# Optimization experiments

Hardware: AMD Instinct MI355X
Metric: run time of the kernel (lower is better)

Reference implementation:

```python
import jax, jax.numpy as jnp
import numpy as np

B, NELEC, D, NION = 2048, 32, 512, 8
NSPIN = 2
N = NELEC // NSPIN  # electrons per spin = orbital-matrix size = 16


def setup_inputs() -> dict:
    key = jax.random.key(0)
    ks = jax.random.split(key, 6)
    eq_inputs = jax.random.normal(ks[0], (B, NELEC, D), jnp.float32)
    r_ei = jax.random.normal(ks[1], (B, NELEC, NION, 3), jnp.float32)
    # learned params (stacked over the 2 spins; equal split so shapes match)
    W_lin = jax.random.normal(ks[2], (NSPIN, 2 * D, N), jnp.float32) * (0.5 / np.sqrt(D))
    b_lin = jax.random.normal(ks[3], (NSPIN, N), jnp.float32) * 0.1
    A_env = jax.random.normal(ks[4], (NSPIN, 3, 3, NION, N), jnp.float32) * 0.3
    w_ion = jax.random.normal(ks[5], (NSPIN, NION, N), jnp.float32)
    return dict(eq_inputs=eq_inputs, r_ei=r_ei, W_lin=W_lin, b_lin=b_lin,
                A_env=A_env, w_ion=w_ion)


def reference(eq_inputs, r_ei, W_lin, b_lin, A_env, w_ion):
    """Per-particle determinant antiequivariance layer.

    For each spin s and particle p, a doubly-equivariant orbital matrix
    M_p[j, k] = (y_p . W1[:,k] + y_j . W2[:,k] + b[k]) * env[j, k]
    is built (pair-concat dense split into two einsums to avoid the (B,n,n,2d)
    intermediate), with anisotropic exponential envelopes
    env[j, k] = sum_I w_ion[I,k] * exp(-||A[:,:,I,k] @ r_ei[j,I,:]||).
    Output per spin: y_p * det(M_p), stacked over spins -> (B, 2, n, d).
    """
    b, nelec, d = eq_inputs.shape
    n = nelec // NSPIN
    x = eq_inputs.reshape(b, NSPIN, n, d)            # spin_split=2 equal split
    r = r_ei.reshape(b, NSPIN, n, r_ei.shape[-2], 3)
    W1, W2 = W_lin[:, :d], W_lin[:, d:]
    # linear (doubly equivariant) part: (B, S, n_p, n_j, n_k)
    lin_p = jnp.einsum('bspf,sfk->bspk', x, W1)
    lin_j = jnp.einsum('bsjf,sfk->bsjk', x, W2) + b_lin[None, :, None, :]
    lin = lin_p[:, :, :, None, :] + lin_j[:, :, None, :, :]
    # anisotropic exponential envelopes: exp(-||A (r - R)||), combined over ions
    ar = jnp.einsum('bsjip,spqik->bsjiqk', r, A_env)        # (B,S,n,I,3,k)
    env = jnp.exp(-jnp.sqrt(jnp.sum(ar * ar, axis=-2)))     # (B,S,n,I,k)
    env = jnp.einsum('bsjik,sik->bsjk', env, w_ion)         # (B,S,n_j,n_k)
    M = lin * env[:, :, None, :, :]                         # (B,S,n_p,n_j,n_k)
    dets = jnp.linalg.det(M)                                # (B,S,n_p)
    # y_p * det(M_p), per spin (stacked over the spin axis)
    return x * dets[..., None]                              # (B,S,n,d)
```

## Files before the change

kernel.cpp:

```cpp
#include <hip/hip_runtime.h>
#include <hip/hip_bf16.h>
#include <cstdint>
#include <cstddef>

#define NSPIN 2
#define NPART 16
#define DDIM  512
#define NION  8

#define WSLICE     976
#define LDS_FLOATS (4 * WSLICE)
#define LDS_BYTES  (LDS_FLOATS * 4)

#define WS_GRAM_F  16384

typedef short bf16x8 __attribute__((ext_vector_type(8)));
typedef float f32x4  __attribute__((ext_vector_type(4)));

__device__ __forceinline__ short bfc(float x) {
    unsigned u = __float_as_uint(x);
    u += 0x7FFFu + ((u >> 16) & 1u);
    return (short)(u >> 16);
}

union AFU { bf16x8 v; __hip_bfloat162 h[4]; };

__device__ __forceinline__ bf16x8 cvt8(const float4& a, const float4& b) {
    AFU u;
    u.h[0] = __float22bfloat162_rn(make_float2(a.x, a.y));
    u.h[1] = __float22bfloat162_rn(make_float2(a.z, a.w));
    u.h[2] = __float22bfloat162_rn(make_float2(b.x, b.y));
    u.h[3] = __float22bfloat162_rn(make_float2(b.z, b.w));
    return u.v;
}

#define DPPMAXU(k, ctrl) { unsigned o_ = (unsigned)__builtin_amdgcn_update_dpp(0, (int)(k), (ctrl), 0xF, 0xF, true); (k) = (k) > o_ ? (k) : o_; }

__global__ void __launch_bounds__(256)
prep_kernel(const float* __restrict__ WL, const float* __restrict__ AE,
            const float* __restrict__ WI, float* __restrict__ WSF)
{
    const int t = threadIdx.x;
    if (blockIdx.x < 16) {
        int slot = blockIdx.x * 256 + t;
        int spin = slot >> 11;
        int rem  = slot & 2047;
        int half = rem >> 10;
        int ks   = (rem >> 6) & 15;
        int lane = rem & 63;
        int cc2  = lane & 15, hh = lane >> 4;
        const float* src = WL + (size_t)spin * (2 * DDIM * NPART)
                         + ((size_t)(half * 512 + ks * 32 + hh * 8)) * NPART + cc2;
        ushort u[8];
        #pragma unroll
        for (int e = 0; e < 8; ++e) u[e] = (ushort)bfc(src[e * NPART]);
        uint4 pk;
        pk.x = (unsigned)u[0] | ((unsigned)u[1] << 16);
        pk.y = (unsigned)u[2] | ((unsigned)u[3] << 16);
        pk.z = (unsigned)u[4] | ((unsigned)u[5] << 16);
        pk.w = (unsigned)u[6] | ((unsigned)u[7] << 16);
        ((uint4*)WSF)[slot] = pk;
    } else {
        int s  = t >> 7;
        int ke = (t >> 3) & 15;
        int i  = t & 7;
        const float* Ag = AE + (size_t)s * (9 * NION * NPART);
        float a00 = Ag[((0 * 3 + 0) * NION + i) * NPART + ke];
        float a01 = Ag[((0 * 3 + 1) * NION + i) * NPART + ke];
        float a02 = Ag[((0 * 3 + 2) * NION + i) * NPART + ke];
        float a10 = Ag[((1 * 3 + 0) * NION + i) * NPART + ke];
        float a11 = Ag[((1 * 3 + 1) * NION + i) * NPART + ke];
        float a12 = Ag[((1 * 3 + 2) * NION + i) * NPART + ke];
        float a20 = Ag[((2 * 3 + 0) * NION + i) * NPART + ke];
        float a21 = Ag[((2 * 3 + 1) * NION + i) * NPART + ke];
        float a22 = Ag[((2 * 3 + 2) * NION + i) * NPART + ke];
        float* g = WSF + WS_GRAM_F + t * 8;
        g[0] = a00 * a00 + a01 * a01 + a02 * a02;
        g[1] = a10 * a10 + a11 * a11 + a12 * a12;
        g[2] = a20 * a20 + a21 * a21 + a22 * a22;
        g[3] = a00 * a10 + a01 * a11 + a02 * a12;
        g[4] = a00 * a20 + a01 * a21 + a02 * a22;
        g[5] = a10 * a20 + a11 * a21 + a12 * a22;
        g[6] = WI[(size_t)s * (NION * NPART) + i * NPART + ke];
        g[7] = 0.f;
    }
}

__global__ void __launch_bounds__(256, 4)
ppdet_kernel(const float* __restrict__ EQ, const float* __restrict__ RE,
             const float* __restrict__ WSF, const float* __restrict__ BL,
             float* __restrict__ OUT)
{
    extern __shared__ float ls[];
    const int t  = threadIdx.x;
    const int s  = blockIdx.x >> 9;
    const int b0 = (blockIdx.x & 511) * 4;

    const int l  = t & 63;
    const int w  = t >> 6;
    const int b  = b0 + w;
    const int c  = l & 15;
    const int h4 = l >> 4;
    const int jr = l & 15;
    const int g  = l >> 4;

    float* wls = ls + w * WSLICE;

    {
        const float* xg  = EQ + ((size_t)(b * 32 + s * 16 + c)) * DDIM + h4 * 8;
        const uint4* wb1 = (const uint4*)WSF + (size_t)s * 2048;
        const uint4* wb2 = wb1 + 1024;
        f32x4 accp = {0.f, 0.f, 0.f, 0.f}, accj = {0.f, 0.f, 0.f, 0.f};
        #pragma unroll
        for (int kb = 0; kb < 4; ++kb) {
            float4 xa[8];
            uint4 w1v[4], w2v[4];
            #pragma unroll
            for (int u = 0; u < 4; ++u) {
                xa[2 * u]     = *(const float4*)(xg + (kb * 4 + u) * 32);
                xa[2 * u + 1] = *(const float4*)(xg + (kb * 4 + u) * 32 + 4);
                w1v[u] = wb1[(kb * 4 + u) * 64 + l];
                w2v[u] = wb2[(kb * 4 + u) * 64 + l];
            }
            #pragma unroll
            for (int u = 0; u < 4; ++u) {
                bf16x8 af = cvt8(xa[2 * u], xa[2 * u + 1]);
                accp = __builtin_amdgcn_mfma_f32_16x16x32_bf16(af, *(bf16x8*)&w1v[u], accp, 0, 0, 0);
                accj = __builtin_amdgcn_mfma_f32_16x16x32_bf16(af, *(bf16x8*)&w2v[u], accj, 0, 0, 0);
            }
        }
        const float blv = BL[s * NPART + c];
        #pragma unroll
        for (int q = 0; q < 4; ++q) {
            wls[(h4 * 4 + q) * 20 + c]        = accp[q];
            wls[320 + (h4 * 4 + q) * 20 + c]  = accj[q] + blv;
        }
    }

    {
        float rr[24];
        const float* rrow = RE + ((size_t)(b * 32 + s * 16 + jr)) * 24;
        #pragma unroll
        for (int m = 0; m < 6; ++m) {
            float4 v = ((const float4*)rrow)[m];
            rr[m * 4 + 0] = v.x; rr[m * 4 + 1] = v.y;
            rr[m * 4 + 2] = v.z; rr[m * 4 + 3] = v.w;
        }
        #pragma unroll
        for (int kx = 0; kx < 4; ++kx) {
            const int ke2 = g + kx * 4;
            const float4* gp = (const float4*)(WSF + WS_GRAM_F + s * 1024 + ke2 * 64);
            float ev = 0.f;
            #pragma unroll
            for (int i = 0; i < 8; ++i) {
                float4 gA = gp[2 * i];
                float4 gB = gp[2 * i + 1];
                float r0 = rr[i * 3 + 0], r1 = rr[i * 3 + 1], r2 = rr[i * 3 + 2];
                float ss = r0 * r0 * gA.x;
                ss = fmaf(r1 * r1, gA.y, ss);
                ss = fmaf(r2 * r2, gA.z, ss);
                float tcr = r0 * r1 * gA.w;
                tcr = fmaf(r0 * r2, gB.x, tcr);
                tcr = fmaf(r1 * r2, gB.y, tcr);
                ss = fmaf(2.f, tcr, ss);
                ss = fmaxf(ss, 0.f);
                ev = fmaf(gB.z, __expf(-__builtin_amdgcn_sqrtf(ss)), ev);
            }
            wls[640 + jr * 20 + ke2] = ev;
        }
    }

    asm volatile("s_waitcnt lgkmcnt(0)" ::: "memory");

    const int lanebase4 = (l & 48) << 2;
    #pragma unroll 1
    for (int pp = 0; pp < 4; ++pp) {
        const int p = pp * 4 + g;
        float Mr[16];
        const float* lp = wls + p * 20;
        const float* lj = wls + 320 + jr * 20;
        const float* ev = wls + 640 + jr * 20;
        #pragma unroll
        for (int cq = 0; cq < 4; ++cq) {
            float4 a  = *(const float4*)(lp + cq * 4);
            float4 bb = *(const float4*)(lj + cq * 4);
            float4 e  = *(const float4*)(ev + cq * 4);
            Mr[cq * 4 + 0] = (a.x + bb.x) * e.x;
            Mr[cq * 4 + 1] = (a.y + bb.y) * e.y;
            Mr[cq * 4 + 2] = (a.z + bb.z) * e.z;
            Mr[cq * 4 + 3] = (a.w + bb.w) * e.w;
        }
        float detv = 1.f;
        unsigned sel = 0u;
        int inv = 0;
        bool msel = false;
        #pragma unroll
        for (int cc = 0; cc < 16; ++cc) {
            unsigned key = msel ? 0u
                : ((__float_as_uint(fabsf(Mr[cc])) & 0xFFFFFFF0u) | (unsigned)jr);
            DPPMAXU(key, 0x121); DPPMAXU(key, 0x122); DPPMAXU(key, 0x124); DPPMAXU(key, 0x128);
            const int idx = (int)(key & 15u);
            const bool ispiv = (jr == idx) && !msel;
            const int srcaddr = lanebase4 | (idx << 2);
            float Pr[16];
            #pragma unroll
            for (int k2 = cc; k2 < 16; ++k2)
                Pr[k2] = __int_as_float(__builtin_amdgcn_ds_bpermute(
                             srcaddr, __float_as_int(Mr[k2])));
            const float pv = Pr[cc];
            const float f = (msel || ispiv || pv == 0.f) ? 0.f
                          : Mr[cc] * __builtin_amdgcn_rcpf(pv);
            inv += __popc(sel >> (idx + 1));
            sel |= (1u << idx);
            msel = msel || ispiv;
            detv *= pv;
            #pragma unroll
            for (int k2 = cc + 1; k2 < 16; ++k2)
                Mr[k2] = fmaf(-f, Pr[k2], Mr[k2]);
        }
        if (inv & 1) detv = -detv;
        if (jr == 0) wls[960 + p] = detv;
    }

    asm volatile("s_waitcnt lgkmcnt(0)" ::: "memory");

    {
        const size_t base = ((size_t)(b * 32 + s * 16)) * DDIM;
        const f32x4* src4 = (const f32x4*)(EQ + base);
        f32x4* dst4 = (f32x4*)(OUT + base);
        #pragma unroll
        for (int i2 = 0; i2 < 32; ++i2) {
            int f4i = i2 * 64 + l;
            float dt = wls[960 + (f4i >> 7)];
            f32x4 xv = src4[f4i];
            f32x4 o = xv * dt;
            __builtin_nontemporal_store(o, dst4 + f4i);
        }
    }
}

extern "C" void kernel_launch(void* const* d_in, const int* in_sizes, int n_in,
                              void* d_out, int out_size, void* d_ws, size_t ws_size,
                              hipStream_t stream) {
    const float* EQ = (const float*)d_in[0];
    const float* RE = (const float*)d_in[1];
    const float* WL = (const float*)d_in[2];
    const float* BL = (const float*)d_in[3];
    const float* AE = (const float*)d_in[4];
    const float* WI = (const float*)d_in[5];
    float* OUT = (float*)d_out;
    float* WSF = (float*)d_ws;
    (void)in_sizes; (void)n_in; (void)out_size; (void)ws_size;

    prep_kernel<<<dim3(17), dim3(256), 0, stream>>>(WL, AE, WI, WSF);
    ppdet_kernel<<<dim3(1024), dim3(256), LDS_BYTES, stream>>>(EQ, RE, WSF, BL, OUT);
}
```

Baseline: 83.53 us.

## Split determinant computation and output scaling into separate kernels

The fused kernel is split in two. The first computes the per-particle determinants and writes them to workspace, and a second fully parallel kernel streams the inputs and scales them into the output. The aim is to decouple the latency-bound elimination phase from the bandwidth-bound scale phase so each gets a better launch shape. The cost is an extra kernel launch and a second full read of the 64MB input, since the fused version could reuse input data that was likely still in cache.

After: 105.8 us. 1.27x slower.

```diff
diff --git a/kernel.cpp b/kernel.cpp
--- a/kernel.cpp
+++ b/kernel.cpp
@@ -13,6 +13,7 @@
 #define LDS_BYTES  (LDS_FLOATS * 4)
 
 #define WS_GRAM_F  16384
+#define WS_DETS_F  18432
 
 typedef short bf16x8 __attribute__((ext_vector_type(8)));
 typedef float f32x4  __attribute__((ext_vector_type(4)));
@@ -87,9 +88,9 @@
 }
 
 __global__ void __launch_bounds__(256, 4)
-ppdet_kernel(const float* __restrict__ EQ, const float* __restrict__ RE,
-             const float* __restrict__ WSF, const float* __restrict__ BL,
-             float* __restrict__ OUT)
+dets_kernel(const float* __restrict__ EQ, const float* __restrict__ RE,
+            const float* __restrict__ WSF, const float* __restrict__ BL,
+            float* __restrict__ DETS)
 {
     extern __shared__ float ls[];
     const int t  = threadIdx.x;
@@ -219,23 +220,24 @@
                 Mr[k2] = fmaf(-f, Pr[k2], Mr[k2]);
         }
         if (inv & 1) detv = -detv;
-        if (jr == 0) wls[960 + p] = detv;
-    }
-
-    asm volatile("s_waitcnt lgkmcnt(0)" ::: "memory");
-
-    {
-        const size_t base = ((size_t)(b * 32 + s * 16)) * DDIM;
-        const f32x4* src4 = (const f32x4*)(EQ + base);
-        f32x4* dst4 = (f32x4*)(OUT + base);
-        #pragma unroll
-        for (int i2 = 0; i2 < 32; ++i2) {
-            int f4i = i2 * 64 + l;
-            float dt = wls[960 + (f4i >> 7)];
-            f32x4 xv = src4[f4i];
-            f32x4 o = xv * dt;
-            __builtin_nontemporal_store(o, dst4 + f4i);
-        }
+        if (jr == 0)
+            DETS[(size_t)(b * 32 + s * 16 + p)] = detv;
+    }
+}
+
+__global__ void __launch_bounds__(256)
+scale_kernel(const float* __restrict__ EQ, const float* __restrict__ DETS,
+             float* __restrict__ OUT)
+{
+    const int tid = blockIdx.x * 256 + threadIdx.x;
+    const f32x4* src = (const f32x4*)EQ;
+    f32x4* dst = (f32x4*)OUT;
+    #pragma unroll
+    for (int it = 0; it < 16; ++it) {
+        const int i = it * 524288 + tid;
+        float dt = DETS[i >> 7];
+        f32x4 v = src[i];
+        __builtin_nontemporal_store(v * dt, dst + i);
     }
 }
 
@@ -253,5 +255,7 @@
     (void)in_sizes; (void)n_in; (void)out_size; (void)ws_size;
 
     prep_kernel<<<dim3(17), dim3(256), 0, stream>>>(WL, AE, WI, WSF);
-    ppdet_kernel<<<dim3(1024), dim3(256), LDS_BYTES, stream>>>(EQ, RE, WSF, BL, OUT);
-}
+    dets_kernel<<<dim3(1024), dim3(256), LDS_BYTES, stream>>>(
+        EQ, RE, WSF, BL, WSF + WS_DETS_F);
+    scale_kernel<<<dim3(2048), dim3(256), 0, stream>>>(EQ, WSF + WS_DETS_F, OUT);
+}
```
